# Kernel optimization log

Hardware: AMD Instinct MI355X
Metric: run time of the kernel (lower is better)

Reference implementation:

```python
import jax, jax.numpy as jnp
import numpy as np

HIDDEN, HEADS, HDIM = 1024, 8, 64
B, S = 4, 8192
LN_EPS = 1e-6


def setup_inputs() -> dict:
    key = jax.random.key(0)
    ks = jax.random.split(key, 12)
    inner = HEADS * HDIM
    sd = HIDDEN ** -0.5
    return {
        "x": jax.random.normal(ks[0], (B, S, HIDDEN), jnp.float32),
        "Wq": jax.random.normal(ks[1], (HIDDEN, inner), jnp.float32) * sd,
        "bq": jnp.zeros((inner,), jnp.float32),
        "Wk": jax.random.normal(ks[2], (HIDDEN, inner), jnp.float32) * sd,
        "bk": jnp.zeros((inner,), jnp.float32),
        "Wv": jax.random.normal(ks[3], (HIDDEN, inner), jnp.float32) * sd,
        "bv": jnp.zeros((inner,), jnp.float32),
        "Wo": jax.random.normal(ks[4], (inner, HIDDEN), jnp.float32) * (inner ** -0.5),
        "bo": jnp.zeros((HIDDEN,), jnp.float32),
        "alpha": jnp.ones((HEADS, HDIM), jnp.float32),
        "aug_param": jax.random.normal(ks[5], (1, HEADS, HDIM), jnp.float32),
        "ln_scale": jnp.ones((HIDDEN,), jnp.float32),
        "ln_bias": jnp.zeros((HIDDEN,), jnp.float32),
    }


def reference(x, Wq, bq, Wk, bk, Wv, bv, Wo, bo, alpha, aug_param, ln_scale, ln_bias):
    b, s, _ = x.shape
    h, d = alpha.shape
    scale = d ** -0.5
    q = (x @ Wq + bq).reshape(b, s, h, d)
    k = (x @ Wk + bk).reshape(b, s, h, d)
    v = (x @ Wv + bv).reshape(b, s, h, d)
    decay = jax.nn.sigmoid(alpha)  # (h, d)

    def step(state, qkv):
        q_t, k_t, v_t = qkv  # each (b, h, d)
        attn = jax.nn.softmax(jnp.einsum('bhd,bhd->bh', q_t, k_t) * scale, axis=-1)
        new_state = decay * state + (1.0 - decay) * attn[..., None] * v_t
        return new_state, new_state

    qs = jnp.moveaxis(q, 1, 0)  # (s, b, h, d)
    ks_ = jnp.moveaxis(k, 1, 0)
    vs = jnp.moveaxis(v, 1, 0)
    init = jnp.zeros((b, h, d), x.dtype)
    _, states = jax.lax.scan(step, init, (qs, ks_, vs))
    states = jnp.moveaxis(states, 0, 1)  # (b, s, h, d)

    aug = jax.nn.sigmoid(q * aug_param)  # aug_param (1,h,d) broadcasts over (b,s,h,d)
    out = (q * states + aug).reshape(b, s, h * d)
    out = out @ Wo + bo
    mean = jnp.mean(out, axis=-1, keepdims=True)
    var = jnp.var(out, axis=-1, keepdims=True)
    return (out - mean) * jax.lax.rsqrt(var + LN_EPS) * ln_scale + ln_bias
```

## Files before the change

kernel.cpp:

```cpp
#include <hip/hip_runtime.h>
#include <hip/hip_bf16.h>


#define HIDDEN 1024
#define HEADS 8
#define HDIM 64
#define INNER 512
#define BATCH 4
#define SEQ 8192
#define ROWS (BATCH*SEQ)
#define NCHUNK 128
#define CHLEN 64

typedef unsigned short u16;
typedef unsigned int u32;
typedef __attribute__((ext_vector_type(8))) short bf16x8;
typedef __attribute__((ext_vector_type(4))) float f32x4;

__device__ __forceinline__ float b2f(u16 u) { return __uint_as_float(((u32)u) << 16); }
__device__ __forceinline__ u16 f2b(float f) {
  u32 u = __float_as_uint(f);
  u32 r = u + 0x7fffu + ((u >> 16) & 1u);
  return (u16)(r >> 16);
}
__device__ __forceinline__ u32 pack2(float a, float b) {
  return (u32)f2b(a) | ((u32)f2b(b) << 16);
}

#define GLOAD_LDS16(gp, lp)                                                  \
  __builtin_amdgcn_global_load_lds(                                          \
      (const __attribute__((address_space(1))) u32*)(gp),                    \
      (__attribute__((address_space(3))) u32*)(lp), 16, 0, 0)

__global__ __launch_bounds__(256) void prep_x(const float* __restrict__ x,
                                              u16* __restrict__ xb) {
  size_t i = ((size_t)blockIdx.x * 256 + threadIdx.x) * 8;
  float4 a = *(const float4*)(x + i);
  float4 b = *(const float4*)(x + i + 4);
  uint4 w = {pack2(a.x, a.y), pack2(a.z, a.w), pack2(b.x, b.y), pack2(b.z, b.w)};
  *(uint4*)(xb + i) = w;
}

__global__ __launch_bounds__(256) void prep_w(
    const float* __restrict__ Wq, const float* __restrict__ Wk,
    const float* __restrict__ Wv, const float* __restrict__ Wo,
    const float* __restrict__ bq, const float* __restrict__ bk,
    const float* __restrict__ bv,
    u16* __restrict__ Wt, u16* __restrict__ Wot, float* __restrict__ bcat) {
  const int WELEM = HIDDEN * INNER;
  int idx = blockIdx.x * 256 + threadIdx.x;
  if (idx < 3 * WELEM) {
    int z = idx / WELEM;
    int rem = idx - z * WELEM;
    int n = rem >> 10;
    int k = rem & 1023;
    const float* W = (z == 0) ? Wq : (z == 1) ? Wk : Wv;
    Wt[idx] = f2b(W[k * INNER + n]);
  } else {
    int rem = idx - 3 * WELEM;
    int n = rem >> 9;
    int k = rem & 511;
    Wot[rem] = f2b(Wo[k * HIDDEN + n]);
  }
  if (idx < 3 * INNER) {
    int z = idx >> 9;
    int n = idx & 511;
    bcat[idx] = (z == 0) ? bq[n] : (z == 1) ? bk[n] : bv[n];
  }
}

template <int K, bool OUT_F32, bool SPLIT3>
__global__ __launch_bounds__(512, 2) void gemm256(
    const u16* __restrict__ A, const u16* __restrict__ Bt,
    const float* __restrict__ bias,
    void* __restrict__ out0, void* __restrict__ out1, void* __restrict__ out2,
    int nTilesN) {
  constexpr int NT = K / 64;
  __shared__ u16 lds[2][32768];

  const int nwg = gridDim.x;
  const int chunk = nwg >> 3;
  const int bid = blockIdx.x;
  const int lin = (bid & 7) * chunk + (bid >> 3);
  const int nt = lin % nTilesN;
  const int mt = lin / nTilesN;
  const int m0 = mt * 256, n0 = nt * 256;
  const int N = nTilesN * 256;

  const int tid = threadIdx.x;
  const int lane = tid & 63;
  const int w = tid >> 6;
  const int wm = w >> 2;
  const int wn = w & 3;
  const int r16 = lane & 15, kq = lane >> 4;

  const int rt = tid >> 3;
  const int cg = (((tid & 7) ^ (rt & 7)) << 3);
  const u16* Ag = A + (size_t)(m0 + rt) * K + cg;
  const u16* Bg = Bt + (size_t)(n0 + rt) * K + cg;
  const int ldst = w * 512;

#define STAGE(buf, kt)                                                          \
  {                                                                             \
    const u16* ga = Ag + (size_t)(kt) * 64;                                     \
    const u16* gb = Bg + (size_t)(kt) * 64;                                     \
    _Pragma("unroll") for (int r = 0; r < 4; r++)                               \
        GLOAD_LDS16(ga + (size_t)r * 64 * K, &lds[buf][r * 4096 + ldst]);       \
    _Pragma("unroll") for (int r = 0; r < 4; r++)                               \
        GLOAD_LDS16(gb + (size_t)r * 64 * K, &lds[buf][16384 + r * 4096 + ldst]); \
  }

  int colx[2];
#pragma unroll
  for (int ks = 0; ks < 2; ks++)
    colx[ks] = (((ks << 5) | (kq << 3)) ^ ((r16 & 7) << 3));
  const int aBase = (wm * 128 + r16) * 64;
  const int bBase = 16384 + (wn * 64 + r16) * 64;

  f32x4 acc[8][4] = {};

#define COMPUTE(buf)                                                           \
  {                                                                            \
    bf16x8 bfr[4][2];                                                          \
    _Pragma("unroll") for (int j = 0; j < 4; j++)                              \
        _Pragma("unroll") for (int ks = 0; ks < 2; ks++)                       \
            bfr[j][ks] = *(const bf16x8*)&lds[buf][bBase + j * 1024 + colx[ks]]; \
    _Pragma("unroll") for (int i = 0; i < 8; i++) {                            \
      bf16x8 a0 = *(const bf16x8*)&lds[buf][aBase + i * 1024 + colx[0]];       \
      bf16x8 a1 = *(const bf16x8*)&lds[buf][aBase + i * 1024 + colx[1]];       \
      _Pragma("unroll") for (int j = 0; j < 4; j++)                            \
          acc[i][j] =                                                          \
          __builtin_amdgcn_mfma_f32_16x16x32_bf16(a0, bfr[j][0], acc[i][j], 0, 0, 0); \
      _Pragma("unroll") for (int j = 0; j < 4; j++)                            \
          acc[i][j] =                                                          \
          __builtin_amdgcn_mfma_f32_16x16x32_bf16(a1, bfr[j][1], acc[i][j], 0, 0, 0); \
    }                                                                          \
  }

  STAGE(0, 0);
  STAGE(1, 1);
  asm volatile("s_waitcnt vmcnt(8)" ::: "memory");
  __builtin_amdgcn_sched_barrier(0);
  __builtin_amdgcn_s_barrier();

  for (int t = 0; t < NT; t += 2) {
    COMPUTE(0);
    asm volatile("s_waitcnt lgkmcnt(0)" ::: "memory");
    __builtin_amdgcn_sched_barrier(0);
    __builtin_amdgcn_s_barrier();
    if (t + 2 < NT) {
      STAGE(0, t + 2);
      asm volatile("s_waitcnt vmcnt(8)" ::: "memory");
    } else {
      asm volatile("s_waitcnt vmcnt(0)" ::: "memory");
    }
    __builtin_amdgcn_sched_barrier(0);
    __builtin_amdgcn_s_barrier();

    COMPUTE(1);
    asm volatile("s_waitcnt lgkmcnt(0)" ::: "memory");
    __builtin_amdgcn_sched_barrier(0);
    __builtin_amdgcn_s_barrier();
    if (t + 3 < NT) {
      STAGE(1, t + 3);
      asm volatile("s_waitcnt vmcnt(8)" ::: "memory");
    } else {
      asm volatile("s_waitcnt vmcnt(0)" ::: "memory");
    }
    __builtin_amdgcn_sched_barrier(0);
    __builtin_amdgcn_s_barrier();
  }
#undef STAGE
#undef COMPUTE

  const int zsel = SPLIT3 ? ((n0 + wn * 64) >> 9) : 0;
  u16* ob16 = (u16*)((zsel == 0) ? out0 : (zsel == 1) ? out1 : out2);
#pragma unroll
  for (int j = 0; j < 4; j++) {
    int col = n0 + wn * 64 + j * 16 + r16;
    float bv = bias[col];
    int colm = SPLIT3 ? (col & 511) : col;
#pragma unroll
    for (int i = 0; i < 8; i++) {
#pragma unroll
      for (int q = 0; q < 4; q++) {
        int row = m0 + wm * 128 + i * 16 + kq * 4 + q;
        float v = acc[i][j][q] + bv;
        if (OUT_F32)
          ((float*)out0)[(size_t)row * N + col] = v;
        else
          ob16[(size_t)row * INNER + colm] = f2b(v);
      }
    }
  }
}

template <bool A_BF16, bool OUT_F32>
__global__ __launch_bounds__(256) void gemm128(
    const void* __restrict__ Aany, const u16* __restrict__ BtBase,
    const float* __restrict__ bias0, const float* __restrict__ bias1,
    const float* __restrict__ bias2,
    void* __restrict__ out0, void* __restrict__ out1, void* __restrict__ out2,
    int K) {
  __shared__ u16 As[128 * 32];
  __shared__ u16 Bs[128 * 32];
  const int N = gridDim.x * 128;
  const int z = blockIdx.z;
  const u16* Bt = BtBase + (size_t)z * N * K;
  const float* bias = (z == 0) ? bias0 : (z == 1) ? bias1 : bias2;
  void* Out = (z == 0) ? out0 : (z == 1) ? out1 : out2;
  const int tid = threadIdx.x;
  const int m0 = blockIdx.y * 128;
  const int n0 = blockIdx.x * 128;
  const int lane = tid & 63;
  const int wid = tid >> 6;
  const int wm = wid >> 1, wn = wid & 1;
  const int r16 = lane & 15, kq = lane >> 4;
  const int r = tid >> 1;
  const int half = tid & 1;
  f32x4 acc[4][4] = {};
  for (int k0 = 0; k0 < K; k0 += 32) {
    __syncthreads();
    if (A_BF16) {
      const u16* Ab = (const u16*)Aany;
      const int4* src = (const int4*)(Ab + (size_t)(m0 + r) * K + k0 + half * 16);
      int4 v0 = src[0];
      int4 v1 = src[1];
      *(int4*)&As[r * 32 + half * 16] = v0;
      *(int4*)&As[r * 32 + half * 16 + 8] = v1;
    } else {
      const float* Af = (const float*)Aany;
      const float4* src = (const float4*)(Af + (size_t)(m0 + r) * K + k0 + half * 16);
      float4 f0 = src[0], f1 = src[1], f2 = src[2], f3 = src[3];
      uint4 w0 = {pack2(f0.x, f0.y), pack2(f0.z, f0.w), pack2(f1.x, f1.y), pack2(f1.z, f1.w)};
      uint4 w1 = {pack2(f2.x, f2.y), pack2(f2.z, f2.w), pack2(f3.x, f3.y), pack2(f3.z, f3.w)};
      *(uint4*)&As[r * 32 + half * 16] = w0;
      *(uint4*)&As[r * 32 + half * 16 + 8] = w1;
    }
    {
      const int4* src = (const int4*)(Bt + (size_t)(n0 + r) * K + k0 + half * 16);
      int4 v0 = src[0];
      int4 v1 = src[1];
      *(int4*)&Bs[r * 32 + half * 16] = v0;
      *(int4*)&Bs[r * 32 + half * 16 + 8] = v1;
    }
    __syncthreads();
    bf16x8 a[4], b[4];
#pragma unroll
    for (int i = 0; i < 4; i++)
      a[i] = *(const bf16x8*)&As[(wm * 64 + i * 16 + r16) * 32 + kq * 8];
#pragma unroll
    for (int j = 0; j < 4; j++)
      b[j] = *(const bf16x8*)&Bs[(wn * 64 + j * 16 + r16) * 32 + kq * 8];
#pragma unroll
    for (int i = 0; i < 4; i++)
#pragma unroll
      for (int j = 0; j < 4; j++)
        acc[i][j] = __builtin_amdgcn_mfma_f32_16x16x32_bf16(a[i], b[j], acc[i][j], 0, 0, 0);
  }
#pragma unroll
  for (int j = 0; j < 4; j++) {
    int col = n0 + wn * 64 + j * 16 + r16;
    float bv = bias[col];
#pragma unroll
    for (int i = 0; i < 4; i++) {
#pragma unroll
      for (int q = 0; q < 4; q++) {
        int row = m0 + wm * 64 + i * 16 + kq * 4 + q;
        float v = acc[i][j][q] + bv;
        if (OUT_F32)
          ((float*)Out)[(size_t)row * N + col] = v;
        else
          ((u16*)Out)[(size_t)row * N + col] = f2b(v);
      }
    }
  }
}

__global__ __launch_bounds__(256) void attn_kernel(
    const u16* __restrict__ qb, const u16* __restrict__ kb,
    float* __restrict__ attn) {
  int lane = threadIdx.x & 63;
  int wid = threadIdx.x >> 6;
  size_t t = (size_t)blockIdx.x * 4 + wid;
  int4 qv = *(const int4*)(qb + t * INNER + lane * 8);
  int4 kv = *(const int4*)(kb + t * INNER + lane * 8);
  const u16* qu = (const u16*)&qv;
  const u16* ku = (const u16*)&kv;
  float s = 0.f;
#pragma unroll
  for (int j = 0; j < 8; j++) s += b2f(qu[j]) * b2f(ku[j]);
  s += __shfl_xor(s, 1);
  s += __shfl_xor(s, 2);
  s += __shfl_xor(s, 4);
  s *= 0.125f;
  float mx = s;
  mx = fmaxf(mx, __shfl_xor(mx, 8));
  mx = fmaxf(mx, __shfl_xor(mx, 16));
  mx = fmaxf(mx, __shfl_xor(mx, 32));
  float e = __expf(s - mx);
  float sm = e;
  sm += __shfl_xor(sm, 8);
  sm += __shfl_xor(sm, 16);
  sm += __shfl_xor(sm, 32);
  float a = e / sm;
  if ((lane & 7) == 0) attn[t * HEADS + (lane >> 3)] = a;
}

__global__ __launch_bounds__(512) void scan_phase1(
    const u16* __restrict__ vb, const float* __restrict__ attn,
    const float* __restrict__ alpha, float* __restrict__ ends) {
  int hd = threadIdx.x;
  int h = hd >> 6;
  int c = blockIdx.x, b = blockIdx.y;
  float decay = 1.f / (1.f + __expf(-alpha[hd]));
  float om = 1.f - decay;
  size_t base = (size_t)b * SEQ + (size_t)c * CHLEN;
  float st = 0.f;
#pragma unroll 8
  for (int i = 0; i < CHLEN; i++) {
    size_t t = base + i;
    float a = attn[t * HEADS + h];
    float v = b2f(vb[t * INNER + hd]);
    st = decay * st + om * a * v;
  }
  ends[((size_t)b * NCHUNK + c) * INNER + hd] = st;
}

__global__ __launch_bounds__(512) void scan_phase2(
    const float* __restrict__ ends, const float* __restrict__ alpha,
    float* __restrict__ carries) {
  int hd = threadIdx.x;
  int b = blockIdx.x;
  float decay = 1.f / (1.f + __expf(-alpha[hd]));
  float dL = __powf(decay, (float)CHLEN);
  float carry = 0.f;
#pragma unroll 8
  for (int c = 0; c < NCHUNK; c++) {
    size_t idx = ((size_t)b * NCHUNK + c) * INNER + hd;
    carries[idx] = carry;
    carry = dL * carry + ends[idx];
  }
}

__global__ __launch_bounds__(512) void scan_phase3(
    const u16* __restrict__ qb, const u16* __restrict__ vb,
    const float* __restrict__ attn, const float* __restrict__ alpha,
    const float* __restrict__ augp, const float* __restrict__ carries,
    u16* __restrict__ outpre) {
  int hd = threadIdx.x;
  int h = hd >> 6;
  int c = blockIdx.x, b = blockIdx.y;
  float decay = 1.f / (1.f + __expf(-alpha[hd]));
  float om = 1.f - decay;
  float ap = augp[hd];
  float st = carries[((size_t)b * NCHUNK + c) * INNER + hd];
  size_t base = (size_t)b * SEQ + (size_t)c * CHLEN;
#pragma unroll 4
  for (int i = 0; i < CHLEN; i++) {
    size_t t = base + i;
    float a = attn[t * HEADS + h];
    float v = b2f(vb[t * INNER + hd]);
    st = decay * st + om * a * v;
    float q = b2f(qb[t * INNER + hd]);
    float aug = 1.f / (1.f + __expf(-q * ap));
    outpre[t * INNER + hd] = f2b(q * st + aug);
  }
}

__global__ __launch_bounds__(256) void ln_kernel(
    float* __restrict__ out, const float* __restrict__ lns,
    const float* __restrict__ lnb) {
  size_t row = blockIdx.x;
  int tid = threadIdx.x;
  float4 v = *(float4*)(out + row * HIDDEN + tid * 4);
  float s = v.x + v.y + v.z + v.w;
  float ss = v.x * v.x + v.y * v.y + v.z * v.z + v.w * v.w;
#pragma unroll
  for (int m = 1; m < 64; m <<= 1) {
    s += __shfl_xor(s, m);
    ss += __shfl_xor(ss, m);
  }
  __shared__ float sb[4], ssb[4];
  int lane = tid & 63, wid = tid >> 6;
  if (lane == 0) {
    sb[wid] = s;
    ssb[wid] = ss;
  }
  __syncthreads();
  s = sb[0] + sb[1] + sb[2] + sb[3];
  ss = ssb[0] + ssb[1] + ssb[2] + ssb[3];
  float mean = s * (1.f / HIDDEN);
  float var = ss * (1.f / HIDDEN) - mean * mean;
  float rstd = rsqrtf(var + 1e-6f);
  float4 sc = *(const float4*)(lns + tid * 4);
  float4 bi = *(const float4*)(lnb + tid * 4);
  v.x = (v.x - mean) * rstd * sc.x + bi.x;
  v.y = (v.y - mean) * rstd * sc.y + bi.y;
  v.z = (v.z - mean) * rstd * sc.z + bi.z;
  v.w = (v.w - mean) * rstd * sc.w + bi.w;
  *(float4*)(out + row * HIDDEN + tid * 4) = v;
}

extern "C" void kernel_launch(void* const* d_in, const int* in_sizes, int n_in,
                              void* d_out, int out_size, void* d_ws, size_t ws_size,
                              hipStream_t stream) {
  const float* x = (const float*)d_in[0];
  const float* Wq = (const float*)d_in[1];
  const float* bq = (const float*)d_in[2];
  const float* Wk = (const float*)d_in[3];
  const float* bk = (const float*)d_in[4];
  const float* Wv = (const float*)d_in[5];
  const float* bv = (const float*)d_in[6];
  const float* Wo = (const float*)d_in[7];
  const float* bo = (const float*)d_in[8];
  const float* alpha = (const float*)d_in[9];
  const float* augp = (const float*)d_in[10];
  const float* lns = (const float*)d_in[11];
  const float* lnb = (const float*)d_in[12];

  char* ws = (char*)d_ws;
  const bool fast = ws_size >= 175118336ull;

  if (fast) {
    u16* xb = (u16*)(ws + 0);
    u16* qb = (u16*)(ws + 67108864);
    u16* kb = (u16*)(ws + 100663296);
    u16* vb = (u16*)(ws + 134217728);
    u16* Wt = (u16*)(ws + 167772160);
    u16* Wot = (u16*)(ws + 170917888);
    float* bcat = (float*)(ws + 171966464);
    float* attn = (float*)(ws + 171972608);
    float* ends = (float*)(ws + 173021184);
    float* car = (float*)(ws + 174069760);
    u16* outpre = kb;

    prep_x<<<ROWS * HIDDEN / 8 / 256, 256, 0, stream>>>(x, xb);
    prep_w<<<8192, 256, 0, stream>>>(Wq, Wk, Wv, Wo, bq, bk, bv, Wt, Wot, bcat);

    gemm256<HIDDEN, false, true><<<768, 512, 0, stream>>>(
        xb, Wt, bcat, qb, kb, vb, 6);

    attn_kernel<<<ROWS / 4, 256, 0, stream>>>(qb, kb, attn);
    scan_phase1<<<dim3(NCHUNK, BATCH), 512, 0, stream>>>(vb, attn, alpha, ends);
    scan_phase2<<<BATCH, 512, 0, stream>>>(ends, alpha, car);
    scan_phase3<<<dim3(NCHUNK, BATCH), 512, 0, stream>>>(qb, vb, attn, alpha, augp, car, outpre);

    gemm256<INNER, true, false><<<512, 512, 0, stream>>>(
        outpre, Wot, bo, d_out, d_out, d_out, 4);

    ln_kernel<<<ROWS, 256, 0, stream>>>((float*)d_out, lns, lnb);
  } else {
    u16* qb = (u16*)(ws + 0);
    u16* kb = (u16*)(ws + 33554432);
    u16* vb = (u16*)(ws + 67108864);
    u16* Wt = (u16*)(ws + 100663296);
    u16* Wot = (u16*)(ws + 103809024);
    float* bcat = (float*)(ws + 104845312);
    float* attn = (float*)(ws + 104857600);
    float* ends = (float*)(ws + 105906176);
    float* car = (float*)(ws + 106954752);
    u16* outpre = kb;

    prep_w<<<8192, 256, 0, stream>>>(Wq, Wk, Wv, Wo, bq, bk, bv, Wt, Wot, bcat);
    gemm128<false, false><<<dim3(4, 256, 3), 256, 0, stream>>>(
        x, Wt, bq, bk, bv, qb, kb, vb, HIDDEN);
    attn_kernel<<<ROWS / 4, 256, 0, stream>>>(qb, kb, attn);
    scan_phase1<<<dim3(NCHUNK, BATCH), 512, 0, stream>>>(vb, attn, alpha, ends);
    scan_phase2<<<BATCH, 512, 0, stream>>>(ends, alpha, car);
    scan_phase3<<<dim3(NCHUNK, BATCH), 512, 0, stream>>>(qb, vb, attn, alpha, augp, car, outpre);
    gemm256<INNER, true, false><<<512, 512, 0, stream>>>(
        outpre, Wot, bo, d_out, d_out, d_out, 4);
    ln_kernel<<<ROWS, 256, 0, stream>>>((float*)d_out, lns, lnb);
  }
}
```

Measured before the change: 327.1 us.

## Replace double-buffered GEMM pipeline with 4-slot ring of K=32 stages

The GEMM kernel's two-buffer, K=64-per-stage pipeline becomes a four-slot ring of K=32 stages with three stages in flight. Each iteration issues the next stage, waits only for the oldest one, and computes on it with a single barrier pair, so global loads overlap MFMA work more deeply. LDS use stays the same and the swizzle is adapted to 32-element rows. The trade-offs are a barrier every 32 K-elements instead of every 64, and a narrower swizzle that may raise LDS bank conflicts.

```diff
diff --git a/kernel.cpp b/kernel.cpp
--- a/kernel.cpp
+++ b/kernel.cpp
@@ -70,13 +70,13 @@
 }
 
 template <int K, bool OUT_F32, bool SPLIT3>
-__global__ __launch_bounds__(512, 2) void gemm256(
+__global__ __launch_bounds__(512, 2) void gemm_ring(
     const u16* __restrict__ A, const u16* __restrict__ Bt,
     const float* __restrict__ bias,
     void* __restrict__ out0, void* __restrict__ out1, void* __restrict__ out2,
     int nTilesN) {
-  constexpr int NT = K / 64;
-  __shared__ u16 lds[2][32768];
+  constexpr int NT = K / 32;
+  __shared__ u16 lds[4][16384];
 
   const int nwg = gridDim.x;
   const int chunk = nwg >> 3;
@@ -94,84 +94,74 @@
   const int wn = w & 3;
   const int r16 = lane & 15, kq = lane >> 4;
 
-  const int rt = tid >> 3;
-  const int cg = (((tid & 7) ^ (rt & 7)) << 3);
+  const int rt = tid >> 2;
+  const int cg = (((tid & 3) ^ (rt & 3)) << 3);
   const u16* Ag = A + (size_t)(m0 + rt) * K + cg;
   const u16* Bg = Bt + (size_t)(n0 + rt) * K + cg;
   const int ldst = w * 512;
 
-#define STAGE(buf, kt)                                                          \
-  {                                                                             \
-    const u16* ga = Ag + (size_t)(kt) * 64;                                     \
-    const u16* gb = Bg + (size_t)(kt) * 64;                                     \
-    _Pragma("unroll") for (int r = 0; r < 4; r++)                               \
-        GLOAD_LDS16(ga + (size_t)r * 64 * K, &lds[buf][r * 4096 + ldst]);       \
-    _Pragma("unroll") for (int r = 0; r < 4; r++)                               \
-        GLOAD_LDS16(gb + (size_t)r * 64 * K, &lds[buf][16384 + r * 4096 + ldst]); \
-  }
-
-  int colx[2];
-#pragma unroll
-  for (int ks = 0; ks < 2; ks++)
-    colx[ks] = (((ks << 5) | (kq << 3)) ^ ((r16 & 7) << 3));
-  const int aBase = (wm * 128 + r16) * 64;
-  const int bBase = 16384 + (wn * 64 + r16) * 64;
+#define STAGE(slot, kt)                                                       \
+  {                                                                           \
+    const u16* ga = Ag + (size_t)(kt) * 32;                                   \
+    const u16* gb = Bg + (size_t)(kt) * 32;                                   \
+    GLOAD_LDS16(ga, &lds[slot][ldst]);                                        \
+    GLOAD_LDS16(ga + (size_t)128 * K, &lds[slot][4096 + ldst]);               \
+    GLOAD_LDS16(gb, &lds[slot][8192 + ldst]);                                 \
+    GLOAD_LDS16(gb + (size_t)128 * K, &lds[slot][12288 + ldst]);              \
+  }
+
+  const int xr = (r16 & 3) << 3;
+  const int aO = (wm * 128 + r16) * 32 + ((kq << 3) ^ xr);
+  const int bO = 8192 + (wn * 64 + r16) * 32 + ((kq << 3) ^ xr);
 
   f32x4 acc[8][4] = {};
 
-#define COMPUTE(buf)                                                           \
+#define COMPUTE(slot)                                                          \
   {                                                                            \
-    bf16x8 bfr[4][2];                                                          \
+    const u16* sl = &lds[slot][0];                                             \
+    bf16x8 af[8], bfv[4];                                                      \
     _Pragma("unroll") for (int j = 0; j < 4; j++)                              \
-        _Pragma("unroll") for (int ks = 0; ks < 2; ks++)                       \
-            bfr[j][ks] = *(const bf16x8*)&lds[buf][bBase + j * 1024 + colx[ks]]; \
-    _Pragma("unroll") for (int i = 0; i < 8; i++) {                            \
-      bf16x8 a0 = *(const bf16x8*)&lds[buf][aBase + i * 1024 + colx[0]];       \
-      bf16x8 a1 = *(const bf16x8*)&lds[buf][aBase + i * 1024 + colx[1]];       \
-      _Pragma("unroll") for (int j = 0; j < 4; j++)                            \
-          acc[i][j] =                                                          \
-          __builtin_amdgcn_mfma_f32_16x16x32_bf16(a0, bfr[j][0], acc[i][j], 0, 0, 0); \
-      _Pragma("unroll") for (int j = 0; j < 4; j++)                            \
-          acc[i][j] =                                                          \
-          __builtin_amdgcn_mfma_f32_16x16x32_bf16(a1, bfr[j][1], acc[i][j], 0, 0, 0); \
-    }                                                                          \
+        bfv[j] = *(const bf16x8*)&sl[bO + j * 512];                            \
+    _Pragma("unroll") for (int i = 0; i < 8; i++)                              \
+        af[i] = *(const bf16x8*)&sl[aO + i * 512];                             \
+    _Pragma("unroll") for (int i = 0; i < 8; i++)                              \
+        _Pragma("unroll") for (int j = 0; j < 4; j++)                          \
+            acc[i][j] =                                                        \
+        __builtin_amdgcn_mfma_f32_16x16x32_bf16(af[i], bfv[j], acc[i][j], 0, 0, 0); \
+  }
+
+#define SYNCB                                                                  \
+  {                                                                            \
+    __builtin_amdgcn_sched_barrier(0);                                         \
+    __builtin_amdgcn_s_barrier();                                              \
+    __builtin_amdgcn_sched_barrier(0);                                         \
   }
 
   STAGE(0, 0);
   STAGE(1, 1);
+  STAGE(2, 2);
+
+  for (int t = 0; t < NT - 3; ++t) {
+    STAGE((t + 3) & 3, t + 3);
+    asm volatile("s_waitcnt vmcnt(12)" ::: "memory");
+    SYNCB;
+    COMPUTE(t & 3);
+    SYNCB;
+  }
   asm volatile("s_waitcnt vmcnt(8)" ::: "memory");
-  __builtin_amdgcn_sched_barrier(0);
-  __builtin_amdgcn_s_barrier();
-
-  for (int t = 0; t < NT; t += 2) {
-    COMPUTE(0);
-    asm volatile("s_waitcnt lgkmcnt(0)" ::: "memory");
-    __builtin_amdgcn_sched_barrier(0);
-    __builtin_amdgcn_s_barrier();
-    if (t + 2 < NT) {
-      STAGE(0, t + 2);
-      asm volatile("s_waitcnt vmcnt(8)" ::: "memory");
-    } else {
-      asm volatile("s_waitcnt vmcnt(0)" ::: "memory");
-    }
-    __builtin_amdgcn_sched_barrier(0);
-    __builtin_amdgcn_s_barrier();
-
-    COMPUTE(1);
-    asm volatile("s_waitcnt lgkmcnt(0)" ::: "memory");
-    __builtin_amdgcn_sched_barrier(0);
-    __builtin_amdgcn_s_barrier();
-    if (t + 3 < NT) {
-      STAGE(1, t + 3);
-      asm volatile("s_waitcnt vmcnt(8)" ::: "memory");
-    } else {
-      asm volatile("s_waitcnt vmcnt(0)" ::: "memory");
-    }
-    __builtin_amdgcn_sched_barrier(0);
-    __builtin_amdgcn_s_barrier();
-  }
+  SYNCB;
+  COMPUTE((NT - 3) & 3);
+  SYNCB;
+  asm volatile("s_waitcnt vmcnt(4)" ::: "memory");
+  SYNCB;
+  COMPUTE((NT - 2) & 3);
+  SYNCB;
+  asm volatile("s_waitcnt vmcnt(0)" ::: "memory");
+  SYNCB;
+  COMPUTE((NT - 1) & 3);
 #undef STAGE
 #undef COMPUTE
+#undef SYNCB
 
   const int zsel = SPLIT3 ? ((n0 + wn * 64) >> 9) : 0;
   u16* ob16 = (u16*)((zsel == 0) ? out0 : (zsel == 1) ? out1 : out2);
@@ -438,7 +428,7 @@
     prep_x<<<ROWS * HIDDEN / 8 / 256, 256, 0, stream>>>(x, xb);
     prep_w<<<8192, 256, 0, stream>>>(Wq, Wk, Wv, Wo, bq, bk, bv, Wt, Wot, bcat);
 
-    gemm256<HIDDEN, false, true><<<768, 512, 0, stream>>>(
+    gemm_ring<HIDDEN, false, true><<<768, 512, 0, stream>>>(
         xb, Wt, bcat, qb, kb, vb, 6);
 
     attn_kernel<<<ROWS / 4, 256, 0, stream>>>(qb, kb, attn);
@@ -446,7 +436,7 @@
     scan_phase2<<<BATCH, 512, 0, stream>>>(ends, alpha, car);
     scan_phase3<<<dim3(NCHUNK, BATCH), 512, 0, stream>>>(qb, vb, attn, alpha, augp, car, outpre);
 
-    gemm256<INNER, true, false><<<512, 512, 0, stream>>>(
+    gemm_ring<INNER, true, false><<<512, 512, 0, stream>>>(
         outpre, Wot, bo, d_out, d_out, d_out, 4);
 
     ln_kernel<<<ROWS, 256, 0, stream>>>((float*)d_out, lns, lnb);
@@ -469,7 +459,7 @@
     scan_phase1<<<dim3(NCHUNK, BATCH), 512, 0, stream>>>(vb, attn, alpha, ends);
     scan_phase2<<<BATCH, 512, 0, stream>>>(ends, alpha, car);
     scan_phase3<<<dim3(NCHUNK, BATCH), 512, 0, stream>>>(qb, vb, attn, alpha, augp, car, outpre);
-    gemm256<INNER, true, false><<<512, 512, 0, stream>>>(
+    gemm_ring<INNER, true, false><<<512, 512, 0, stream>>>(
         outpre, Wot, bo, d_out, d_out, d_out, 4);
     ln_kernel<<<ROWS, 256, 0, stream>>>((float*)d_out, lns, lnb);
   }
```

Result: no change. 324.1 us (-0.9%).
